# Kernel optimization log

Hardware: AMD Instinct MI355X
Metric: run time of the kernel (lower is better)

## Reference

```python
import jax, jax.numpy as jnp
import numpy as np

ITERS = 10   # self.iters
REG = 0.1    # self.reg
EPS = 1e-12  # F.normalize eps


def setup_inputs() -> dict:
    key = jax.random.key(0)
    k1, k2 = jax.random.split(key)
    b, n_s, h = 64, 512, 1024
    x = jax.random.normal(k1, (b, n_s, h), dtype=jnp.float32)
    y = jax.random.normal(k2, (b, n_s, h), dtype=jnp.float32)
    return {"x": x, "y": y}


def _l2_normalize(t):
    n = jnp.sqrt(jnp.sum(t * t, axis=-1, keepdims=True))
    return t / jnp.maximum(n, EPS)


def reference(x, y):
    # CosineScorer.score(x, y, get_diag=False) with temperature=1
    xn = _l2_normalize(x)
    yn = _l2_normalize(y)
    scores = jnp.einsum('bmh,bnh->bmn', xn, yn)  # (b, n_s, n_s)
    b, m, n = scores.shape

    # uniform log marginals: -log(n_s)
    log_mu = jnp.full((b, m), -jnp.log(jnp.float32(m)), dtype=scores.dtype)
    log_nu = jnp.full((b, n), -jnp.log(jnp.float32(n)), dtype=scores.dtype)

    # log_ipot: iterative proximal point OT in log space
    A = scores / jnp.float32(REG)

    def step(carry, _):
        v, T = carry
        Q = A + T                                              # (b, m, n)
        u = log_mu - jax.nn.logsumexp(Q + v[:, None, :], axis=2)
        v_new = log_nu - jax.nn.logsumexp(Q + u[:, :, None], axis=1)
        T_new = Q + u[:, :, None] + v_new[:, None, :]
        return (v_new, T_new), None

    init = (log_nu, jnp.zeros_like(scores))
    (_, T), _ = jax.lax.scan(step, init, None, length=ITERS)

    matching = jnp.exp(T)
    return jnp.sum(scores * matching, axis=(1, 2))  # (b,)
```

## Files before the change

### kernel.cpp

```cpp
#include <hip/hip_runtime.h>
#include <hip/hip_fp16.h>

#define NB 64
#define NS 512
#define NH 1024
#define NITERS 10

#define LOG_INV_NS (-6.238324625039508f)

using half8 = _Float16 __attribute__((ext_vector_type(8)));
using f32x4 = float __attribute__((ext_vector_type(4)));

__global__ __launch_bounds__(512) void gemm_fused(
    const float* __restrict__ x, const float* __restrict__ y,
    _Float16* __restrict__ Sh) {
  __shared__ _Float16 As[2][256][40];
  __shared__ _Float16 Bs[2][256][40];
  __shared__ float invA[256], invB[256];

  int blk = blockIdx.x;
  int b = blk & 63;
  int tile = blk >> 6;
  int tm = (tile >> 1) * 256, tn = (tile & 1) * 256;
  int tid = threadIdx.x;
  int wid = tid >> 6, lane = tid & 63;
  int wr = (wid >> 2) * 128;
  int wc = (wid & 3) * 64;
  int fr = lane & 15, fq = lane >> 4;

  int srow = tid >> 1;
  int skh = (tid & 1) * 16;
  const float* xb = x + ((size_t)b * NS + tm + srow) * NH + skh;
  const float* yb = y + ((size_t)b * NS + tn + srow) * NH + skh;

  f32x4 acc[8][4] = {};
  float4 rx[4], ry[4];
  float sqx = 0.f, sqy = 0.f;

#define GLOAD(K0)                                                     \
  do {                                                                \
    const float4* px = (const float4*)(xb + (K0));                    \
    const float4* py = (const float4*)(yb + (K0));                    \
    rx[0] = px[0]; rx[1] = px[1]; rx[2] = px[2]; rx[3] = px[3];       \
    ry[0] = py[0]; ry[1] = py[1]; ry[2] = py[2]; ry[3] = py[3];       \
  } while (0)

#define CAST_WRITE(BUF)                                               \
  do {                                                                \
    alignas(16) _Float16 ta[16];                                      \
    alignas(16) _Float16 tb[16];                                      \
    _Pragma("unroll") for (int j = 0; j < 4; ++j) {                   \
      float4 v = rx[j];                                               \
      ta[4 * j + 0] = (_Float16)v.x;                                  \
      ta[4 * j + 1] = (_Float16)v.y;                                  \
      ta[4 * j + 2] = (_Float16)v.z;                                  \
      ta[4 * j + 3] = (_Float16)v.w;                                  \
      sqx += v.x * v.x + v.y * v.y + v.z * v.z + v.w * v.w;           \
    }                                                                 \
    _Pragma("unroll") for (int j = 0; j < 4; ++j) {                   \
      float4 v = ry[j];                                               \
      tb[4 * j + 0] = (_Float16)v.x;                                  \
      tb[4 * j + 1] = (_Float16)v.y;                                  \
      tb[4 * j + 2] = (_Float16)v.z;                                  \
      tb[4 * j + 3] = (_Float16)v.w;                                  \
      sqy += v.x * v.x + v.y * v.y + v.z * v.z + v.w * v.w;           \
    }                                                                 \
    *(half8*)&As[BUF][srow][skh + 0] = *(half8*)&ta[0];               \
    *(half8*)&As[BUF][srow][skh + 8] = *(half8*)&ta[8];               \
    *(half8*)&Bs[BUF][srow][skh + 0] = *(half8*)&tb[0];               \
    *(half8*)&Bs[BUF][srow][skh + 8] = *(half8*)&tb[8];               \
  } while (0)

  GLOAD(0);
  CAST_WRITE(0);
  GLOAD(32);

  for (int s = 0; s < 32; ++s) {
    __syncthreads();
    int cur = s & 1;
    if (s < 31) {
      CAST_WRITE(cur ^ 1);
      if (s < 30) GLOAD((s + 2) * 32);
    }
    half8 bf[4];
#pragma unroll
    for (int j = 0; j < 4; ++j)
      bf[j] = *(const half8*)&Bs[cur][wc + 16 * j + fr][8 * fq];
#pragma unroll
    for (int i = 0; i < 8; ++i) {
      half8 af = *(const half8*)&As[cur][wr + 16 * i + fr][8 * fq];
#pragma unroll
      for (int j = 0; j < 4; ++j)
        acc[i][j] = __builtin_amdgcn_mfma_f32_16x16x32_f16(af, bf[j], acc[i][j], 0, 0, 0);
    }
  }
#undef GLOAD
#undef CAST_WRITE

  sqx += __shfl_xor(sqx, 1, 64);
  sqy += __shfl_xor(sqy, 1, 64);
  if ((tid & 1) == 0) {
    invA[srow] = 1.0f / fmaxf(sqrtf(sqx), 1e-12f);
    invB[srow] = 1.0f / fmaxf(sqrtf(sqy), 1e-12f);
  }
  __syncthreads();

  _Float16* Sb = Sh + (size_t)b * NS * NS;
#pragma unroll
  for (int i = 0; i < 8; ++i)
#pragma unroll
    for (int j = 0; j < 4; ++j) {
      int rr = wr + 16 * i + 4 * fq;
      int cc = wc + 16 * j + fr;
      float ib = invB[cc];
#pragma unroll
      for (int p = 0; p < 4; ++p)
        Sb[(size_t)(tm + rr + p) * NS + tn + cc] =
            (_Float16)(acc[i][j][p] * invA[rr + p] * ib);
    }
}

__global__ __launch_bounds__(256) void init_kernel(float* __restrict__ V, float* __restrict__ W) {
  int i = blockIdx.x * 256 + threadIdx.x;
  V[i] = 0.f;
  W[i] = LOG_INV_NS;
}

__global__ __launch_bounds__(256) void u_kernel(
    const _Float16* __restrict__ Sh, const float* __restrict__ W,
    float* __restrict__ U, float f) {
  __shared__ float Wt[8][65];
  int blk = blockIdx.x;
  int bs = blk & 7, rest = blk >> 3;
  int rowgrp = rest & 31, bq = rest >> 5;
  int b = bq * 8 + bs;
  int t = threadIdx.x;
#pragma unroll
  for (int i = 0; i < 2; ++i) {
    int idx = t + 256 * i;
    Wt[idx & 7][idx >> 3] = W[b * NS + idx];
  }
  __syncthreads();
  int w = t >> 6, l = t & 63;
  float wn[8];
#pragma unroll
  for (int e = 0; e < 8; ++e) wn[e] = Wt[e][l];
  int m0 = rowgrp * 16 + w * 4;
  const _Float16* Sb = Sh + ((size_t)b * NS + m0) * NS + 8 * l;
  float sum[4] = {0.f, 0.f, 0.f, 0.f};
#pragma unroll
  for (int k = 0; k < 4; ++k) {
    half8 hv = *(const half8*)(Sb + (size_t)k * NS);
#pragma unroll
    for (int e = 0; e < 8; ++e) sum[k] += __expf(fmaf(f, (float)hv[e], wn[e]));
  }
#pragma unroll
  for (int o = 32; o; o >>= 1) {
#pragma unroll
    for (int k = 0; k < 4; ++k) sum[k] += __shfl_xor(sum[k], o, 64);
  }
  if (l == 0) {
#pragma unroll
    for (int k = 0; k < 4; ++k)
      U[b * NS + m0 + k] = LOG_INV_NS - __logf(sum[k]);
  }
}

__global__ __launch_bounds__(256) void v_kernel(
    const _Float16* __restrict__ Sh, const float* __restrict__ U,
    float* __restrict__ V, float* __restrict__ W,
    float f, int last, float* __restrict__ outPart) {
  __shared__ float Ul[NS];
  __shared__ float partC[16][128];
  __shared__ float partD[16][128];
  __shared__ float red[128];
  int blk = blockIdx.x;
  int bs = blk & 7, rest = blk >> 3;
  int q = rest & 3, bq = rest >> 2;
  int b = bq * 8 + bs;
  int t = threadIdx.x;
  Ul[t] = U[b * NS + t];
  Ul[t + 256] = U[b * NS + t + 256];
  __syncthreads();

  int r = t >> 4, cg = t & 15;
  const _Float16* Sb = Sh + (size_t)b * NS * NS + q * 128 + cg * 8;
  float c[8] = {}, d[8] = {};
  if (!last) {
#pragma unroll 4
    for (int s = 0; s < 32; ++s) {
      int m = s * 16 + r;
      half8 hv = *(const half8*)(Sb + (size_t)m * NS);
      float um = Ul[m];
#pragma unroll
      for (int e = 0; e < 8; ++e) c[e] += __expf(fmaf(f, (float)hv[e], um));
    }
  } else {
#pragma unroll 2
    for (int s = 0; s < 32; ++s) {
      int m = s * 16 + r;
      half8 hv = *(const half8*)(Sb + (size_t)m * NS);
      float um = Ul[m];
#pragma unroll
      for (int e = 0; e < 8; ++e) {
        float sv = (float)hv[e];
        float ev = __expf(fmaf(f, sv, um));
        c[e] += ev;
        d[e] = fmaf(sv, ev, d[e]);
      }
    }
  }
  *(f32x4*)&partC[r][cg * 8 + 0] = f32x4{c[0], c[1], c[2], c[3]};
  *(f32x4*)&partC[r][cg * 8 + 4] = f32x4{c[4], c[5], c[6], c[7]};
  if (last) {
    *(f32x4*)&partD[r][cg * 8 + 0] = f32x4{d[0], d[1], d[2], d[3]};
    *(f32x4*)&partD[r][cg * 8 + 4] = f32x4{d[4], d[5], d[6], d[7]};
  }
  __syncthreads();
  if (t < 128) {
    float ct = 0.f;
#pragma unroll
    for (int r2 = 0; r2 < 16; ++r2) ct += partC[r2][t];
    float vnew = LOG_INV_NS - __logf(ct);
    int n = b * NS + q * 128 + t;
    float vold = V[n];
    V[n] = vnew;
    W[n] = 2.f * vnew - vold;
    if (last) {
      float dt = 0.f;
#pragma unroll
      for (int r2 = 0; r2 < 16; ++r2) dt += partD[r2][t];
      red[t] = dt / ct;
    }
  }
  if (last) {
    __syncthreads();
    for (int s2 = 64; s2 > 0; s2 >>= 1) {
      if (t < s2) red[t] += red[t + s2];
      __syncthreads();
    }
    if (t == 0) outPart[b * 4 + q] = red[0] * (1.0f / (float)NS);
  }
}

__global__ void combine_kernel(const float* __restrict__ outPart, float* __restrict__ out) {
  int b = threadIdx.x;
  out[b] = outPart[4 * b] + outPart[4 * b + 1] + outPart[4 * b + 2] + outPart[4 * b + 3];
}

extern "C" void kernel_launch(void* const* d_in, const int* in_sizes, int n_in,
                              void* d_out, int out_size, void* d_ws, size_t ws_size,
                              hipStream_t stream) {
  (void)in_sizes; (void)n_in; (void)out_size; (void)ws_size;
  const float* x = (const float*)d_in[0];
  const float* y = (const float*)d_in[1];
  float* out = (float*)d_out;

  char* ws = (char*)d_ws;
  _Float16* Sh = (_Float16*)ws;
  float* fregion = (float*)(ws + (size_t)NB * NS * NS * 2);
  float* U = fregion;
  float* V = U + NB * NS;
  float* W = V + NB * NS;
  float* outPart = W + NB * NS;

  gemm_fused<<<256, 512, 0, stream>>>(x, y, Sh);
  init_kernel<<<(NB * NS) / 256, 256, 0, stream>>>(V, W);

  for (int t = 1; t <= NITERS; ++t) {
    float f = 10.0f * (float)t;
    u_kernel<<<2048, 256, 0, stream>>>(Sh, W, U, f);
    v_kernel<<<256, 256, 0, stream>>>(Sh, U, V, W, f, t == NITERS ? 1 : 0, outPart);
  }
  combine_kernel<<<1, 64, 0, stream>>>(outPart, out);
}
```

Baseline: 222.2 us.

## Split v_kernel across 1024 blocks with 32-column slices and shuffle reductions

The column logsumexp kernel is re-partitioned. Each block now handles 32 columns of one batch instead of 128, so the grid grows from 256 to 1024 blocks. Each thread reads 8 rows by 8 columns, and partial sums are reduced through padded shared memory and wavefront shuffles in place of the serial tree reduction. The point is to fill more compute units and cut per-block reduction latency on the V pass. In exchange, every iteration now computes the d accumulator even when it is not needed, and the final output needs 16 partials per batch.

Measured after the change: 214.0 us. 1.04x faster.

```diff
diff --git a/kernel.cpp b/kernel.cpp
--- a/kernel.cpp
+++ b/kernel.cpp
@@ -51,18 +51,14 @@
     alignas(16) _Float16 tb[16];                                      \
     _Pragma("unroll") for (int j = 0; j < 4; ++j) {                   \
       float4 v = rx[j];                                               \
-      ta[4 * j + 0] = (_Float16)v.x;                                  \
-      ta[4 * j + 1] = (_Float16)v.y;                                  \
-      ta[4 * j + 2] = (_Float16)v.z;                                  \
-      ta[4 * j + 3] = (_Float16)v.w;                                  \
+      ta[4 * j + 0] = (_Float16)v.x; ta[4 * j + 1] = (_Float16)v.y;   \
+      ta[4 * j + 2] = (_Float16)v.z; ta[4 * j + 3] = (_Float16)v.w;   \
       sqx += v.x * v.x + v.y * v.y + v.z * v.z + v.w * v.w;           \
     }                                                                 \
     _Pragma("unroll") for (int j = 0; j < 4; ++j) {                   \
       float4 v = ry[j];                                               \
-      tb[4 * j + 0] = (_Float16)v.x;                                  \
-      tb[4 * j + 1] = (_Float16)v.y;                                  \
-      tb[4 * j + 2] = (_Float16)v.z;                                  \
-      tb[4 * j + 3] = (_Float16)v.w;                                  \
+      tb[4 * j + 0] = (_Float16)v.x; tb[4 * j + 1] = (_Float16)v.y;   \
+      tb[4 * j + 2] = (_Float16)v.z; tb[4 * j + 3] = (_Float16)v.w;   \
       sqy += v.x * v.x + v.y * v.y + v.z * v.z + v.w * v.w;           \
     }                                                                 \
     *(half8*)&As[BUF][srow][skh + 0] = *(half8*)&ta[0];               \
@@ -171,81 +167,80 @@
     float* __restrict__ V, float* __restrict__ W,
     float f, int last, float* __restrict__ outPart) {
   __shared__ float Ul[NS];
-  __shared__ float partC[16][128];
-  __shared__ float partD[16][128];
-  __shared__ float red[128];
+  __shared__ float partC[64][33];
+  __shared__ float partD[64][33];
+  __shared__ float redC[4][33];
+  __shared__ float redD[4][33];
   int blk = blockIdx.x;
-  int bs = blk & 7, rest = blk >> 3;
-  int q = rest & 3, bq = rest >> 2;
-  int b = bq * 8 + bs;
+  int b = blk & 63;
+  int ng = blk >> 6;
   int t = threadIdx.x;
   Ul[t] = U[b * NS + t];
   Ul[t + 256] = U[b * NS + t + 256];
   __syncthreads();
 
-  int r = t >> 4, cg = t & 15;
-  const _Float16* Sb = Sh + (size_t)b * NS * NS + q * 128 + cg * 8;
+  int oct = t & 3;
+  int mc = t >> 2;
+  const _Float16* Sb = Sh + (size_t)b * NS * NS + (size_t)(mc * 8) * NS + ng * 32 + oct * 8;
   float c[8] = {}, d[8] = {};
-  if (!last) {
-#pragma unroll 4
-    for (int s = 0; s < 32; ++s) {
-      int m = s * 16 + r;
-      half8 hv = *(const half8*)(Sb + (size_t)m * NS);
-      float um = Ul[m];
-#pragma unroll
-      for (int e = 0; e < 8; ++e) c[e] += __expf(fmaf(f, (float)hv[e], um));
-    }
-  } else {
-#pragma unroll 2
-    for (int s = 0; s < 32; ++s) {
-      int m = s * 16 + r;
-      half8 hv = *(const half8*)(Sb + (size_t)m * NS);
-      float um = Ul[m];
-#pragma unroll
-      for (int e = 0; e < 8; ++e) {
-        float sv = (float)hv[e];
-        float ev = __expf(fmaf(f, sv, um));
-        c[e] += ev;
-        d[e] = fmaf(sv, ev, d[e]);
-      }
-    }
-  }
-  *(f32x4*)&partC[r][cg * 8 + 0] = f32x4{c[0], c[1], c[2], c[3]};
-  *(f32x4*)&partC[r][cg * 8 + 4] = f32x4{c[4], c[5], c[6], c[7]};
-  if (last) {
-    *(f32x4*)&partD[r][cg * 8 + 0] = f32x4{d[0], d[1], d[2], d[3]};
-    *(f32x4*)&partD[r][cg * 8 + 4] = f32x4{d[4], d[5], d[6], d[7]};
-  }
-  __syncthreads();
-  if (t < 128) {
-    float ct = 0.f;
-#pragma unroll
-    for (int r2 = 0; r2 < 16; ++r2) ct += partC[r2][t];
-    float vnew = LOG_INV_NS - __logf(ct);
-    int n = b * NS + q * 128 + t;
+#pragma unroll
+  for (int i = 0; i < 8; ++i) {
+    half8 hv = *(const half8*)(Sb + (size_t)i * NS);
+    float um = Ul[mc * 8 + i];
+#pragma unroll
+    for (int e = 0; e < 8; ++e) {
+      float sv = (float)hv[e];
+      float ev = __expf(fmaf(f, sv, um));
+      c[e] += ev;
+      d[e] = fmaf(sv, ev, d[e]);
+    }
+  }
+#pragma unroll
+  for (int e = 0; e < 8; ++e) {
+    partC[mc][oct * 8 + e] = c[e];
+    partD[mc][oct * 8 + e] = d[e];
+  }
+  __syncthreads();
+  {
+    int ci = t & 31, seg = t >> 5;
+    float cc = 0.f, dd = 0.f;
+#pragma unroll
+    for (int k = 0; k < 8; ++k) {
+      cc += partC[seg * 8 + k][ci];
+      dd += partD[seg * 8 + k][ci];
+    }
+    cc += __shfl_xor(cc, 32, 64);
+    dd += __shfl_xor(dd, 32, 64);
+    int w = t >> 6, l = t & 63;
+    if (l < 32) { redC[w][l] = cc; redD[w][l] = dd; }
+  }
+  __syncthreads();
+  if (t < 32) {
+    float cc = redC[0][t] + redC[1][t] + redC[2][t] + redC[3][t];
+    float vnew = LOG_INV_NS - __logf(cc);
+    int n = b * NS + ng * 32 + t;
     float vold = V[n];
     V[n] = vnew;
     W[n] = 2.f * vnew - vold;
     if (last) {
-      float dt = 0.f;
-#pragma unroll
-      for (int r2 = 0; r2 < 16; ++r2) dt += partD[r2][t];
-      red[t] = dt / ct;
-    }
-  }
-  if (last) {
-    __syncthreads();
-    for (int s2 = 64; s2 > 0; s2 >>= 1) {
-      if (t < s2) red[t] += red[t + s2];
-      __syncthreads();
-    }
-    if (t == 0) outPart[b * 4 + q] = red[0] * (1.0f / (float)NS);
+      float dd = redD[0][t] + redD[1][t] + redD[2][t] + redD[3][t];
+      float r = dd / cc;
+      r += __shfl_xor(r, 16, 64);
+      r += __shfl_xor(r, 8, 64);
+      r += __shfl_xor(r, 4, 64);
+      r += __shfl_xor(r, 2, 64);
+      r += __shfl_xor(r, 1, 64);
+      if (t == 0) outPart[b * 16 + ng] = r * (1.0f / (float)NS);
+    }
   }
 }
 
 __global__ void combine_kernel(const float* __restrict__ outPart, float* __restrict__ out) {
   int b = threadIdx.x;
-  out[b] = outPart[4 * b] + outPart[4 * b + 1] + outPart[4 * b + 2] + outPart[4 * b + 3];
+  float s = 0.f;
+#pragma unroll
+  for (int k = 0; k < 16; ++k) s += outPart[b * 16 + k];
+  out[b] = s;
 }
 
 extern "C" void kernel_launch(void* const* d_in, const int* in_sizes, int n_in,
@@ -270,7 +265,7 @@
   for (int t = 1; t <= NITERS; ++t) {
     float f = 10.0f * (float)t;
     u_kernel<<<2048, 256, 0, stream>>>(Sh, W, U, f);
-    v_kernel<<<256, 256, 0, stream>>>(Sh, U, V, W, f, t == NITERS ? 1 : 0, outPart);
+    v_kernel<<<1024, 256, 0, stream>>>(Sh, U, V, W, f, t == NITERS ? 1 : 0, outPart);
   }
   combine_kernel<<<1, 64, 0, stream>>>(outPart, out);
 }
```
